# Optimization experiments

Hardware: AMD Instinct MI355X
Metric: run time of the kernel (lower is better)

## Reference

```python
import jax, jax.numpy as jnp
import numpy as np
from jax import lax


def setup_inputs() -> dict:
    key = jax.random.key(0)
    k1, k2 = jax.random.split(key)
    X = jax.random.normal(k1, (32, 64, 112, 112), dtype=jnp.float32)
    # module draws K ~ N(0, 0.01) each forward; we materialize it as a param
    K = 0.01 * jax.random.normal(k2, (128, 64, 3, 3), dtype=jnp.float32)
    return {"X": X, "K": K}


def reference(X, K):
    # Valid-padding cross-correlation, NCHW input, OIHW kernel, no bias.
    # Matches conv2d_multi_out: sum over in_channels, stack over out_channels.
    return lax.conv_general_dilated(
        X, K,
        window_strides=(1, 1),
        padding="VALID",
        dimension_numbers=("NCHW", "OIHW", "NCHW"),
    )
```

## Files before the change

kernel.cpp:

```cpp
#include <hip/hip_runtime.h>


typedef __attribute__((ext_vector_type(8)))  _Float16 f16x8;
typedef __attribute__((ext_vector_type(16))) float    f32x16;

typedef __attribute__((address_space(3))) uint       lds_u32;
typedef __attribute__((address_space(1))) const uint glb_u32;

constexpr int C_IN = 64, H = 112, W = 112;
constexpr int COUT = 128, OH = 110, OW = 110;
constexpr int NIMG = 32;
constexpr int KTOT = C_IN * 9;
constexpr int OSP  = OH * OW;
constexpr int SPTOT = NIMG * OSP;
constexpr int IMG_STRIDE = C_IN * H * W;
constexpr int CH_STRIDE  = H * W;
constexpr size_t A16_BYTES = (size_t)KTOT * COUT * 2;

__device__ __forceinline__ uint pkrtz_u32(float lo, float hi) {
    union { __fp16 __attribute__((ext_vector_type(2))) h; uint u; } c;
    c.h = __builtin_amdgcn_cvt_pkrtz(lo, hi);
    return c.u;
}

__global__ void prep_a(const float* __restrict__ Kw, _Float16* __restrict__ A16) {
    int idx = blockIdx.x * 256 + threadIdx.x;
    if (idx >= COUT * KTOT) return;
    int cout = idx / KTOT, k = idx - cout * KTOT;
    int c = k / 9, s = k - c * 9;
    int o = c >> 3, j = c & 7;
    A16[((size_t)(s * 8 + o) * COUT + cout) * 8 + j] = (_Float16)Kw[idx];
}

__global__ __launch_bounds__(256, 4)
void prep_x(const float* __restrict__ X, _Float16* __restrict__ X16t) {
    __shared__ _Float16 L[W * 72];
    const int t = threadIdx.x;
    const int n = blockIdx.x / H, h = blockIdx.x - n * H;
    const float* src = X + (size_t)n * IMG_STRIDE + (size_t)h * W;
    const int c = t >> 2, q = t & 3;
    const float* sc = src + (size_t)c * CH_STRIDE + q * 28;
#pragma unroll
    for (int v = 0; v < 7; v++) {
        float4 f = *reinterpret_cast<const float4*>(sc + v * 4);
        const int w0 = q * 28 + v * 4;
        L[(w0 + 0) * 72 + c] = (_Float16)f.x;
        L[(w0 + 1) * 72 + c] = (_Float16)f.y;
        L[(w0 + 2) * 72 + c] = (_Float16)f.z;
        L[(w0 + 3) * 72 + c] = (_Float16)f.w;
    }
    __syncthreads();
    _Float16* dst = X16t + ((size_t)n * H + h) * W * 64;
#pragma unroll
    for (int r = 0; r < 4; r++) {
        const int u = r * 256 + t;
        if (u < 896) {
            const int w = u >> 3, sl = u & 7;
            *reinterpret_cast<f16x8*>(dst + (size_t)u * 8) =
                *reinterpret_cast<const f16x8*>(&L[w * 72 + sl * 8]);
        }
    }
}

__global__ __launch_bounds__(512, 4)
void conv_v12(const _Float16* __restrict__ X16t,
              const _Float16* __restrict__ A16,
              float* __restrict__ Out)
{
    __shared__ __align__(16) _Float16 Bs[2][128 * 64];

    const int t = threadIdx.x;

    const int nwg = gridDim.x;
    const int q8 = nwg >> 3, r8 = nwg & 7;
    const int xcd = blockIdx.x & 7, idx8 = blockIdx.x >> 3;
    const int bid = (xcd < r8 ? xcd * (q8 + 1) : r8 * (q8 + 1) + (xcd - r8) * q8) + idx8;
    const int spBase = bid * 128;

    const int lane = t & 63;
    const int wv   = t >> 6;
    const int u0 = wv * 128 + lane;
    const int u1 = u0 + 64;
    const _Float16* s0;
    const _Float16* s1;
    {
        const int uu[2] = {u0, u1};
        const _Float16* ss[2];
#pragma unroll
        for (int i = 0; i < 2; i++) {
            const int u  = uu[i];
            const int sp = u >> 3, slot = u & 7;
            const int spg = spBase + sp;
            const int n   = spg / OSP;
            const int r   = spg - n * OSP;
            const int oh  = r / OW;
            const int ow  = r - oh * OW;
            ss[i] = X16t + (((size_t)n * H + oh) * W + ow) * 64 + (slot ^ (sp & 7)) * 8;
        }
        s0 = ss[0]; s1 = ss[1];
    }
    const int l0 = u0 * 8;
    const int l1 = u1 * 8;

    const int wq    = wv >> 1;
    const int wc    = wv & 1;
    const int frow  = lane & 31;
    const int khalf = lane >> 5;
    const size_t arow = (size_t)(wq * 32 + frow) * 8;
    const int bmask = frow & 7;
    const int brw0  = (wc * 64 + frow) * 64;
    const int brw1  = brw0 + 32 * 64;

    f32x16 acc[2];
#pragma unroll
    for (int j = 0; j < 2; j++)
#pragma unroll
        for (int e = 0; e < 16; e++) acc[j][e] = 0.f;

    f16x8 aA[4], aB[4];

#define SOFFC(S) ((((S) / 3) * W + ((S) % 3)) * 64)

#define STAGE(S, B)                                                            \
    {                                                                          \
        __builtin_amdgcn_global_load_lds((const glb_u32*)(s0 + SOFFC(S)),      \
                                         (lds_u32*)(&Bs[B][l0]), 16, 0, 0);    \
        __builtin_amdgcn_global_load_lds((const glb_u32*)(s1 + SOFFC(S)),      \
                                         (lds_u32*)(&Bs[B][l1]), 16, 0, 0);    \
    }

#define ALOAD(DST, S)                                                          \
    {                                                                          \
        _Pragma("unroll")                                                      \
        for (int kk = 0; kk < 4; kk++)                                         \
            DST[kk] = *reinterpret_cast<const f16x8*>(                         \
                &A16[(size_t)(((S) * 8 + kk * 2 + khalf) * COUT) * 8 + arow]); \
    }

#define MFMA_STEP(B, AREG)                                                     \
    {                                                                          \
        _Pragma("unroll")                                                      \
        for (int kk = 0; kk < 4; kk++) {                                       \
            const int slot = ((kk * 2 + khalf) ^ bmask) * 8;                   \
            f16x8 b0 = *reinterpret_cast<const f16x8*>(&Bs[B][brw0 + slot]);   \
            f16x8 b1 = *reinterpret_cast<const f16x8*>(&Bs[B][brw1 + slot]);   \
            acc[0] = __builtin_amdgcn_mfma_f32_32x32x16_f16(AREG[kk], b0, acc[0], 0, 0, 0); \
            acc[1] = __builtin_amdgcn_mfma_f32_32x32x16_f16(AREG[kk], b1, acc[1], 0, 0, 0); \
        }                                                                      \
    }

#define STEP(S, CUR, NXT)                                                      \
    {                                                                          \
        ALOAD(NXT, (S) + 1);                                                   \
        STAGE((S) + 1, ((S) + 1) & 1);                                         \
        MFMA_STEP((S) & 1, CUR);                                               \
        __syncthreads();                                                       \
    }

    ALOAD(aA, 0);
    STAGE(0, 0);
    __syncthreads();

    STEP(0, aA, aB);
    STEP(1, aB, aA);
    STEP(2, aA, aB);
    STEP(3, aB, aA);
    STEP(4, aA, aB);
    STEP(5, aB, aA);
    STEP(6, aA, aB);
    STEP(7, aB, aA);
    MFMA_STEP(0, aA);

#undef STAGE
#undef ALOAD
#undef MFMA_STEP
#undef STEP
#undef SOFFC

#pragma unroll
    for (int j = 0; j < 2; j++) {
        const int sp2 = spBase + wc * 64 + j * 32 + frow;
        const int n2  = sp2 / OSP;
        const int r2  = sp2 - n2 * OSP;
        float* Ob = Out + (size_t)n2 * (COUT * (size_t)OSP) + r2;
        const int cbase = wq * 32 + 4 * khalf;
#pragma unroll
        for (int reg = 0; reg < 16; reg++) {
            const int crow = cbase + (reg & 3) + 8 * (reg >> 2);
            Ob[(size_t)crow * OSP] = acc[j][reg];
        }
    }
}

extern "C" void kernel_launch(void* const* d_in, const int* in_sizes, int n_in,
                              void* d_out, int out_size, void* d_ws, size_t ws_size,
                              hipStream_t stream) {
    const float* X  = (const float*)d_in[0];
    const float* Kw = (const float*)d_in[1];
    float* Out = (float*)d_out;
    _Float16* A16  = (_Float16*)d_ws;
    _Float16* X16t = (_Float16*)((char*)d_ws + A16_BYTES);

    prep_a<<<(COUT * KTOT + 255) / 256, 256, 0, stream>>>(Kw, A16);
    prep_x<<<NIMG * H, 256, 0, stream>>>(X, X16t);
    conv_v12<<<SPTOT / 128, 512, 0, stream>>>(X16t, A16, Out);
}
```

Measured before the change: 122.5 us.

## Stage one contiguous input row window per kernel row and reuse across horizontal taps

Instead of gathering a fresh 128-pixel tile from global memory for each of the 9 filter taps, each block loads a contiguous 136-pixel window of the NHWC fp16 input once per kernel row. The three horizontal taps then read that window at shifted offsets. This cuts global-to-LDS traffic and barrier count from 9 stages to 3. The cost is extra index math, a segment split for tiles that cross an image boundary, and a third partial load done by one wave. The slightly larger LDS buffer may affect occupancy.

```diff
diff --git a/kernel.cpp b/kernel.cpp
--- a/kernel.cpp
+++ b/kernel.cpp
@@ -15,6 +15,9 @@
 constexpr int SPTOT = NIMG * OSP;
 constexpr int IMG_STRIDE = C_IN * H * W;
 constexpr int CH_STRIDE  = H * W;
+constexpr int XROW = W * C_IN;
+constexpr int SLOTS = 136;
+constexpr int UNITS = SLOTS * 8;
 constexpr size_t A16_BYTES = (size_t)KTOT * COUT * 2;
 
 __device__ __forceinline__ uint pkrtz_u32(float lo, float hi) {
@@ -50,7 +53,7 @@
         L[(w0 + 3) * 72 + c] = (_Float16)f.w;
     }
     __syncthreads();
-    _Float16* dst = X16t + ((size_t)n * H + h) * W * 64;
+    _Float16* dst = X16t + ((size_t)n * H + h) * XROW;
 #pragma unroll
     for (int r = 0; r < 4; r++) {
         const int u = r * 256 + t;
@@ -63,11 +66,11 @@
 }
 
 __global__ __launch_bounds__(512, 4)
-void conv_v12(const _Float16* __restrict__ X16t,
+void conv_v13(const _Float16* __restrict__ X16t,
               const _Float16* __restrict__ A16,
               float* __restrict__ Out)
 {
-    __shared__ __align__(16) _Float16 Bs[2][128 * 64];
+    __shared__ __align__(16) _Float16 Bs[2][SLOTS * 64];
 
     const int t = threadIdx.x;
 
@@ -77,39 +80,59 @@
     const int bid = (xcd < r8 ? xcd * (q8 + 1) : r8 * (q8 + 1) + (xcd - r8) * q8) + idx8;
     const int spBase = bid * 128;
 
+    const int n0  = spBase / OSP;
+    const int r0  = spBase - n0 * OSP;
+    const int oh0 = r0 / OW;
+    const int ow0 = r0 - oh0 * OW;
+    const int seg1len = (109 - oh0) * 112 + (112 - ow0);
+
     const int lane = t & 63;
     const int wv   = t >> 6;
-    const int u0 = wv * 128 + lane;
-    const int u1 = u0 + 64;
-    const _Float16* s0;
-    const _Float16* s1;
+    const _Float16* sU0;
+    const _Float16* sU1;
+    const _Float16* sU2;
     {
-        const int uu[2] = {u0, u1};
-        const _Float16* ss[2];
-#pragma unroll
-        for (int i = 0; i < 2; i++) {
+        const int uu[3] = {t, t + 512, 1024 + (t & 63)};
+        const _Float16* ss[3];
+#pragma unroll
+        for (int i = 0; i < 3; i++) {
             const int u  = uu[i];
-            const int sp = u >> 3, slot = u & 7;
-            const int spg = spBase + sp;
-            const int n   = spg / OSP;
-            const int r   = spg - n * OSP;
-            const int oh  = r / OW;
-            const int ow  = r - oh * OW;
-            ss[i] = X16t + (((size_t)n * H + oh) * W + ow) * 64 + (slot ^ (sp & 7)) * 8;
-        }
-        s0 = ss[0]; s1 = ss[1];
-    }
-    const int l0 = u0 * 8;
-    const int l1 = u1 * 8;
+            const int ws = u >> 3, oct = u & 7;
+            const int so = (oct ^ (ws & 7)) * 8;
+            size_t lin;
+            if (ws < seg1len) {
+                lin = (size_t)n0 * CH_STRIDE + (size_t)(oh0 * 112 + ow0 + ws);
+            } else {
+                const int nn = (n0 < NIMG - 1) ? n0 + 1 : n0;
+                lin = (size_t)nn * CH_STRIDE + (size_t)(ws - seg1len);
+            }
+            ss[i] = X16t + lin * 64 + so;
+        }
+        sU0 = ss[0]; sU1 = ss[1]; sU2 = ss[2];
+    }
 
     const int wq    = wv >> 1;
     const int wc    = wv & 1;
     const int frow  = lane & 31;
     const int khalf = lane >> 5;
     const size_t arow = (size_t)(wq * 32 + frow) * 8;
-    const int bmask = frow & 7;
-    const int brw0  = (wc * 64 + frow) * 64;
-    const int brw1  = brw0 + 32 * 64;
+
+    int w0i, w1i;
+    {
+        const int ii[2] = {wc * 64 + frow, wc * 64 + 32 + frow};
+        int wx[2];
+#pragma unroll
+        for (int i = 0; i < 2; i++) {
+            const int spg = spBase + ii[i];
+            const int n   = spg / OSP;
+            const int r   = spg - n * OSP;
+            const int oh  = r / OW;
+            const int ow  = r - oh * OW;
+            wx[i] = (n == n0) ? (oh - oh0) * 112 + (ow - ow0)
+                              : seg1len + oh * 112 + ow;
+        }
+        w0i = wx[0]; w1i = wx[1];
+    }
 
     f32x16 acc[2];
 #pragma unroll
@@ -119,14 +142,15 @@
 
     f16x8 aA[4], aB[4];
 
-#define SOFFC(S) ((((S) / 3) * W + ((S) % 3)) * 64)
-
-#define STAGE(S, B)                                                            \
+#define STAGE(R, B)                                                            \
     {                                                                          \
-        __builtin_amdgcn_global_load_lds((const glb_u32*)(s0 + SOFFC(S)),      \
-                                         (lds_u32*)(&Bs[B][l0]), 16, 0, 0);    \
-        __builtin_amdgcn_global_load_lds((const glb_u32*)(s1 + SOFFC(S)),      \
-                                         (lds_u32*)(&Bs[B][l1]), 16, 0, 0);    \
+        __builtin_amdgcn_global_load_lds((const glb_u32*)(sU0 + (R) * XROW),   \
+            (lds_u32*)(&Bs[B][(size_t)t * 8]), 16, 0, 0);                      \
+        __builtin_amdgcn_global_load_lds((const glb_u32*)(sU1 + (R) * XROW),   \
+            (lds_u32*)(&Bs[B][(size_t)(t + 512) * 8]), 16, 0, 0);              \
+        if (wv == 0)                                                           \
+            __builtin_amdgcn_global_load_lds((const glb_u32*)(sU2 + (R) * XROW), \
+                (lds_u32*)(&Bs[B][(size_t)(1024 + lane) * 8]), 16, 0, 0);      \
     }
 
 #define ALOAD(DST, S)                                                          \
@@ -137,45 +161,45 @@
                 &A16[(size_t)(((S) * 8 + kk * 2 + khalf) * COUT) * 8 + arow]); \
     }
 
-#define MFMA_STEP(B, AREG)                                                     \
+#define MFMA_SH(KW, B, AREG)                                                   \
     {                                                                          \
+        const int sa = w0i + (KW);                                             \
+        const int sb = w1i + (KW);                                             \
         _Pragma("unroll")                                                      \
         for (int kk = 0; kk < 4; kk++) {                                       \
-            const int slot = ((kk * 2 + khalf) ^ bmask) * 8;                   \
-            f16x8 b0 = *reinterpret_cast<const f16x8*>(&Bs[B][brw0 + slot]);   \
-            f16x8 b1 = *reinterpret_cast<const f16x8*>(&Bs[B][brw1 + slot]);   \
+            const int oct = kk * 2 + khalf;                                    \
+            f16x8 b0 = *reinterpret_cast<const f16x8*>(                        \
+                &Bs[B][sa * 64 + ((oct ^ (sa & 7)) << 3)]);                    \
+            f16x8 b1 = *reinterpret_cast<const f16x8*>(                        \
+                &Bs[B][sb * 64 + ((oct ^ (sb & 7)) << 3)]);                    \
             acc[0] = __builtin_amdgcn_mfma_f32_32x32x16_f16(AREG[kk], b0, acc[0], 0, 0, 0); \
             acc[1] = __builtin_amdgcn_mfma_f32_32x32x16_f16(AREG[kk], b1, acc[1], 0, 0, 0); \
         }                                                                      \
     }
 
-#define STEP(S, CUR, NXT)                                                      \
-    {                                                                          \
-        ALOAD(NXT, (S) + 1);                                                   \
-        STAGE((S) + 1, ((S) + 1) & 1);                                         \
-        MFMA_STEP((S) & 1, CUR);                                               \
-        __syncthreads();                                                       \
-    }
-
     ALOAD(aA, 0);
     STAGE(0, 0);
     __syncthreads();
 
-    STEP(0, aA, aB);
-    STEP(1, aB, aA);
-    STEP(2, aA, aB);
-    STEP(3, aB, aA);
-    STEP(4, aA, aB);
-    STEP(5, aB, aA);
-    STEP(6, aA, aB);
-    STEP(7, aB, aA);
-    MFMA_STEP(0, aA);
+    STAGE(1, 1);
+    ALOAD(aB, 1); MFMA_SH(0, 0, aA);
+    ALOAD(aA, 2); MFMA_SH(1, 0, aB);
+    ALOAD(aB, 3); MFMA_SH(2, 0, aA);
+    __syncthreads();
+
+    STAGE(2, 0);
+    ALOAD(aA, 4); MFMA_SH(0, 1, aB);
+    ALOAD(aB, 5); MFMA_SH(1, 1, aA);
+    ALOAD(aA, 6); MFMA_SH(2, 1, aB);
+    __syncthreads();
+
+    ALOAD(aB, 7); MFMA_SH(0, 0, aA);
+    ALOAD(aA, 8); MFMA_SH(1, 0, aB);
+    MFMA_SH(2, 0, aA);
 
 #undef STAGE
 #undef ALOAD
-#undef MFMA_STEP
-#undef STEP
-#undef SOFFC
+#undef MFMA_SH
 
 #pragma unroll
     for (int j = 0; j < 2; j++) {
@@ -203,5 +227,5 @@
 
     prep_a<<<(COUT * KTOT + 255) / 256, 256, 0, stream>>>(Kw, A16);
     prep_x<<<NIMG * H, 256, 0, stream>>>(X, X16t);
-    conv_v12<<<SPTOT / 128, 512, 0, stream>>>(X16t, A16, Out);
-}
+    conv_v13<<<SPTOT / 128, 512, 0, stream>>>(X16t, A16, Out);
+}
```

Result: faster. 118.8 us (-3.0%).
